# Optimization experiments

Hardware: AMD Instinct MI355X
Metric: run time of the kernel (lower is better)

## Reference

```python
import jax, jax.numpy as jnp
import numpy as np

A_VOCAB = 400000   # embedding table rows (a)
D = 200            # embedding_dim, hard-coded as 200 in the original module
C = 50000          # number of concepts
T = 1000000        # total flattened ancestor entries (~20 per concept)
B = 1024           # batch of input vectors x


def setup_inputs() -> dict:
    key = jax.random.key(0)
    k1, k2, k3, k4 = jax.random.split(key, 4)
    return {
        "x": jax.random.normal(k1, (B, D), dtype=jnp.float32),
        "embed_weight": jax.random.normal(k2, (A_VOCAB, D), dtype=jnp.float32) * 0.02,
        "ancestor_ids": jax.random.randint(k3, (T,), 0, A_VOCAB, dtype=jnp.int32),
        "segment_ids": jnp.sort(jax.random.randint(k4, (T,), 0, C, dtype=jnp.int32)),
        "n_concepts": C,
    }


def reference(x, embed_weight, ancestor_ids, segment_ids, n_concepts):
    # Ragged gather + per-concept sum (the original's Python loop over concepts)
    gathered = embed_weight[ancestor_ids]                                   # [T, D]
    local_H = jax.ops.segment_sum(gathered, segment_ids,
                                  num_segments=n_concepts)                  # [C, D]
    # concept_vector = local_H @ x.T ; output = softmax(concept_vector.T, dim=1)
    logits = jnp.einsum('bd,cd->bc', x, local_H)                            # [B, C]
    return jax.nn.softmax(logits, axis=1)
```

## Files before the change

kernel.cpp:

```cpp
#include <hip/hip_runtime.h>
#include <hip/hip_bf16.h>

#define DDIM   200
#define CSEG   50000
#define TTOT   1000000
#define BROWS  1024
#define KPAD   224
#define NTILE  64
#define NT     782
#define NPAD   50048
#define MTILES 8

typedef __attribute__((ext_vector_type(8))) __bf16 bf16x8;
typedef __attribute__((ext_vector_type(4))) float  f32x4;
typedef unsigned short u16;

#define WS_XB    0
#define WS_HB    458752
#define WS_PART  (458752 + 22421504)
#define WS_INV   (458752 + 22421504 + 3203072)
#define WS_START (458752 + 22421504 + 3203072 + 4096)

__device__ inline u16 f2bf(float f) {
  unsigned u = __float_as_uint(f);
  u += 0x7FFFu + ((u >> 16) & 1u);
  return (u16)(u >> 16);
}

__global__ __launch_bounds__(64) void prep_x_kernel(const float* __restrict__ x,
                                                    u16* __restrict__ xb) {
  const int row = blockIdx.x;
  const int lane = threadIdx.x;
  if (lane >= 56) return;
  const int col = lane * 4;
  ushort4 o = make_ushort4(0, 0, 0, 0);
  if (col < DDIM) {
    const float4 v = *reinterpret_cast<const float4*>(x + (size_t)row * DDIM + col);
    o = make_ushort4(f2bf(v.x), f2bf(v.y), f2bf(v.z), f2bf(v.w));
  }
  *reinterpret_cast<ushort4*>(xb + (size_t)row * KPAD + col) = o;
}

__global__ __launch_bounds__(256) void seg_start_kernel(const int* __restrict__ sid,
                                                        int* __restrict__ start) {
  const int t = blockIdx.x * 256 + threadIdx.x;
  if (t >= TTOT) return;
  const int cur = sid[t];
  const int prev = (t == 0) ? -1 : sid[t - 1];
  for (int c = prev + 1; c <= cur; ++c) start[c] = t;
  if (t == TTOT - 1) {
    for (int c = cur + 1; c <= CSEG; ++c) start[c] = TTOT;
  }
}

__global__ __launch_bounds__(256) void seg_sum_kernel(const float* __restrict__ embed,
                                                      const int* __restrict__ aid,
                                                      const int* __restrict__ start,
                                                      u16* __restrict__ Hb) {
  const int wave = threadIdx.x >> 6;
  const int lane = threadIdx.x & 63;
  const int c = blockIdx.x * 4 + wave;
  if (c >= NPAD || lane >= 56) return;
  const int col = lane * 4;
  const bool act = (col < DDIM);
  float4 a0 = {0.f, 0.f, 0.f, 0.f}, a1 = a0, a2 = a0, a3 = a0;
  if (c < CSEG && act) {
    const int s = start[c], e = start[c + 1];
    int t = s;
    for (; t + 4 <= e; t += 4) {
      const int i0 = aid[t], i1 = aid[t + 1], i2 = aid[t + 2], i3 = aid[t + 3];
      const float4 v0 = *reinterpret_cast<const float4*>(embed + (size_t)i0 * DDIM + col);
      const float4 v1 = *reinterpret_cast<const float4*>(embed + (size_t)i1 * DDIM + col);
      const float4 v2 = *reinterpret_cast<const float4*>(embed + (size_t)i2 * DDIM + col);
      const float4 v3 = *reinterpret_cast<const float4*>(embed + (size_t)i3 * DDIM + col);
      a0.x += v0.x; a0.y += v0.y; a0.z += v0.z; a0.w += v0.w;
      a1.x += v1.x; a1.y += v1.y; a1.z += v1.z; a1.w += v1.w;
      a2.x += v2.x; a2.y += v2.y; a2.z += v2.z; a2.w += v2.w;
      a3.x += v3.x; a3.y += v3.y; a3.z += v3.z; a3.w += v3.w;
    }
    for (; t < e; ++t) {
      const int i0 = aid[t];
      const float4 v0 = *reinterpret_cast<const float4*>(embed + (size_t)i0 * DDIM + col);
      a0.x += v0.x; a0.y += v0.y; a0.z += v0.z; a0.w += v0.w;
    }
    a0.x += a1.x + a2.x + a3.x;
    a0.y += a1.y + a2.y + a3.y;
    a0.z += a1.z + a2.z + a3.z;
    a0.w += a1.w + a2.w + a3.w;
  }
  const ushort4 o = make_ushort4(f2bf(a0.x), f2bf(a0.y), f2bf(a0.z), f2bf(a0.w));
  *reinterpret_cast<ushort4*>(Hb + (size_t)c * KPAD + col) =
      (c < CSEG && act) ? o : make_ushort4(0, 0, 0, 0);
}

__device__ inline void gemm_tile(const u16* __restrict__ xb, const u16* __restrict__ Hb,
                                 int m0, int n0, int lane, f32x4 acc[2][4]) {
  const int r  = lane & 15;
  const int ko = (lane >> 4) * 8;
  const u16* xp = xb + (size_t)(m0 + r) * KPAD + ko;
  const u16* hp = Hb + (size_t)(n0 + r) * KPAD + ko;
  for (int ks = 0; ks < KPAD / 32; ++ks) {
    const int kb = ks * 32;
    const bf16x8 a0 = *reinterpret_cast<const bf16x8*>(xp + kb);
    const bf16x8 a1 = *reinterpret_cast<const bf16x8*>(xp + 16 * KPAD + kb);
#pragma unroll
    for (int ni = 0; ni < 4; ++ni) {
      const bf16x8 b = *reinterpret_cast<const bf16x8*>(hp + (size_t)ni * 16 * KPAD + kb);
      acc[0][ni] = __builtin_amdgcn_mfma_f32_16x16x32_bf16(a0, b, acc[0][ni], 0, 0, 0);
      acc[1][ni] = __builtin_amdgcn_mfma_f32_16x16x32_bf16(a1, b, acc[1][ni], 0, 0, 0);
    }
  }
}

__global__ __launch_bounds__(256) void gemm_pass1_kernel(const u16* __restrict__ xb,
                                                         const u16* __restrict__ Hb,
                                                         float* __restrict__ partials) {
  const int ntile = blockIdx.x, mtile = blockIdx.y;
  const int lane = threadIdx.x & 63, wave = threadIdx.x >> 6;
  const int m0 = mtile * 128 + wave * 32;
  const int n0 = ntile * NTILE;
  f32x4 acc[2][4] = {};
  gemm_tile(xb, Hb, m0, n0, lane, acc);
  const int cbase = n0 + (lane & 15);
#pragma unroll
  for (int mi = 0; mi < 2; ++mi) {
#pragma unroll
    for (int rr = 0; rr < 4; ++rr) {
      float s = 0.f;
#pragma unroll
      for (int ni = 0; ni < 4; ++ni) {
        if (cbase + ni * 16 < CSEG) s += __expf(acc[mi][ni][rr]);
      }
      for (int off = 1; off < 16; off <<= 1) s += __shfl_xor(s, off, 64);
      if ((lane & 15) == 0) {
        const int row = m0 + mi * 16 + (lane >> 4) * 4 + rr;
        partials[(size_t)row * NT + ntile] = s;
      }
    }
  }
}

__global__ __launch_bounds__(256) void reduce_kernel(const float* __restrict__ partials,
                                                     float* __restrict__ invs) {
  const int row = blockIdx.x, tid = threadIdx.x;
  float s = 0.f;
  for (int nt = tid; nt < NT; nt += 256) s += partials[(size_t)row * NT + nt];
  __shared__ float sm[256];
  sm[tid] = s;
  __syncthreads();
  for (int st = 128; st > 0; st >>= 1) {
    if (tid < st) sm[tid] += sm[tid + st];
    __syncthreads();
  }
  if (tid == 0) invs[row] = 1.0f / sm[0];
}

__global__ __launch_bounds__(256) void gemm_pass2_kernel(const u16* __restrict__ xb,
                                                         const u16* __restrict__ Hb,
                                                         const float* __restrict__ invs,
                                                         float* __restrict__ out) {
  const int ntile = blockIdx.x, mtile = blockIdx.y;
  const int lane = threadIdx.x & 63, wave = threadIdx.x >> 6;
  const int m0 = mtile * 128 + wave * 32;
  const int n0 = ntile * NTILE;
  f32x4 acc[2][4] = {};
  gemm_tile(xb, Hb, m0, n0, lane, acc);
  const int c0 = n0 + (lane & 15);
#pragma unroll
  for (int mi = 0; mi < 2; ++mi) {
#pragma unroll
    for (int rr = 0; rr < 4; ++rr) {
      const int row = m0 + mi * 16 + (lane >> 4) * 4 + rr;
      const float inv = invs[row];
      float* orow = out + (size_t)row * CSEG;
#pragma unroll
      for (int ni = 0; ni < 4; ++ni) {
        const int col = c0 + ni * 16;
        if (col < CSEG) orow[col] = __expf(acc[mi][ni][rr]) * inv;
      }
    }
  }
}

extern "C" void kernel_launch(void* const* d_in, const int* in_sizes, int n_in,
                              void* d_out, int out_size, void* d_ws, size_t ws_size,
                              hipStream_t stream) {
  const float* x     = (const float*)d_in[0];
  const float* embed = (const float*)d_in[1];
  const int*   aid   = (const int*)d_in[2];
  const int*   sid   = (const int*)d_in[3];

  char* ws = (char*)d_ws;
  u16*   xb       = (u16*)(ws + WS_XB);
  u16*   Hb       = (u16*)(ws + WS_HB);
  float* partials = (float*)(ws + WS_PART);
  float* invs     = (float*)(ws + WS_INV);
  int*   start    = (int*)(ws + WS_START);
  float* out      = (float*)d_out;

  hipLaunchKernelGGL(prep_x_kernel,     dim3(BROWS),            dim3(64),  0, stream, x, xb);
  hipLaunchKernelGGL(seg_start_kernel,  dim3((TTOT + 255) / 256), dim3(256), 0, stream, sid, start);
  hipLaunchKernelGGL(seg_sum_kernel,    dim3(NPAD / 4),         dim3(256), 0, stream, embed, aid, start, Hb);
  hipLaunchKernelGGL(gemm_pass1_kernel, dim3(NT, MTILES),       dim3(256), 0, stream, xb, Hb, partials);
  hipLaunchKernelGGL(reduce_kernel,     dim3(BROWS),            dim3(256), 0, stream, partials, invs);
  hipLaunchKernelGGL(gemm_pass2_kernel, dim3(NT, MTILES),       dim3(256), 0, stream, xb, Hb, invs, out);
}
```

Baseline: 325.9 us.

## Fuse prep kernels, widen gather unroll, remap GEMM blocks, nontemporal output stores

Merges the x-to-bf16 conversion and the segment-start computation into one launch. The segment-sum gather is unrolled to eight masked loads in flight to add memory-level parallelism. GEMM blocks are remapped over a 1-D grid so that consecutive blocks spread across M tiles in an XCD-aware order. Pass-2 writes its output with nontemporal stores to avoid cache pollution. The masked loads spend extra bandwidth on tail iterations, and the remap may hurt L2 reuse of H tiles.

```diff
diff --git a/kernel.cpp b/kernel.cpp
--- a/kernel.cpp
+++ b/kernel.cpp
@@ -10,6 +10,7 @@
 #define NT     782
 #define NPAD   50048
 #define MTILES 8
+#define GEMM_BLOCKS (NT * MTILES)
 
 typedef __attribute__((ext_vector_type(8))) __bf16 bf16x8;
 typedef __attribute__((ext_vector_type(4))) float  f32x4;
@@ -27,29 +28,28 @@
   return (u16)(u >> 16);
 }
 
-__global__ __launch_bounds__(64) void prep_x_kernel(const float* __restrict__ x,
-                                                    u16* __restrict__ xb) {
-  const int row = blockIdx.x;
-  const int lane = threadIdx.x;
-  if (lane >= 56) return;
-  const int col = lane * 4;
-  ushort4 o = make_ushort4(0, 0, 0, 0);
-  if (col < DDIM) {
-    const float4 v = *reinterpret_cast<const float4*>(x + (size_t)row * DDIM + col);
-    o = make_ushort4(f2bf(v.x), f2bf(v.y), f2bf(v.z), f2bf(v.w));
-  }
-  *reinterpret_cast<ushort4*>(xb + (size_t)row * KPAD + col) = o;
-}
-
-__global__ __launch_bounds__(256) void seg_start_kernel(const int* __restrict__ sid,
-                                                        int* __restrict__ start) {
-  const int t = blockIdx.x * 256 + threadIdx.x;
-  if (t >= TTOT) return;
-  const int cur = sid[t];
-  const int prev = (t == 0) ? -1 : sid[t - 1];
-  for (int c = prev + 1; c <= cur; ++c) start[c] = t;
-  if (t == TTOT - 1) {
-    for (int c = cur + 1; c <= CSEG; ++c) start[c] = TTOT;
+__global__ __launch_bounds__(256) void fused_prep_kernel(const int* __restrict__ sid,
+                                                         int* __restrict__ start,
+                                                         const float* __restrict__ x,
+                                                         u16* __restrict__ xb) {
+  const int gtid = blockIdx.x * 256 + threadIdx.x;
+  if (gtid < TTOT) {
+    const int cur = sid[gtid];
+    const int prev = (gtid == 0) ? -1 : sid[gtid - 1];
+    for (int c = prev + 1; c <= cur; ++c) start[c] = gtid;
+    if (gtid == TTOT - 1) {
+      for (int c = cur + 1; c <= CSEG; ++c) start[c] = TTOT;
+    }
+  }
+  if (gtid < BROWS * 56) {
+    const int row = gtid / 56;
+    const int col = (gtid % 56) * 4;
+    ushort4 o = make_ushort4(0, 0, 0, 0);
+    if (col < DDIM) {
+      const float4 v = *reinterpret_cast<const float4*>(x + (size_t)row * DDIM + col);
+      o = make_ushort4(f2bf(v.x), f2bf(v.y), f2bf(v.z), f2bf(v.w));
+    }
+    *reinterpret_cast<ushort4*>(xb + (size_t)row * KPAD + col) = o;
   }
 }
 
@@ -63,34 +63,51 @@
   if (c >= NPAD || lane >= 56) return;
   const int col = lane * 4;
   const bool act = (col < DDIM);
-  float4 a0 = {0.f, 0.f, 0.f, 0.f}, a1 = a0, a2 = a0, a3 = a0;
+  float4 a[8];
+#pragma unroll
+  for (int j = 0; j < 8; ++j) a[j] = make_float4(0.f, 0.f, 0.f, 0.f);
   if (c < CSEG && act) {
     const int s = start[c], e = start[c + 1];
-    int t = s;
-    for (; t + 4 <= e; t += 4) {
-      const int i0 = aid[t], i1 = aid[t + 1], i2 = aid[t + 2], i3 = aid[t + 3];
-      const float4 v0 = *reinterpret_cast<const float4*>(embed + (size_t)i0 * DDIM + col);
-      const float4 v1 = *reinterpret_cast<const float4*>(embed + (size_t)i1 * DDIM + col);
-      const float4 v2 = *reinterpret_cast<const float4*>(embed + (size_t)i2 * DDIM + col);
-      const float4 v3 = *reinterpret_cast<const float4*>(embed + (size_t)i3 * DDIM + col);
-      a0.x += v0.x; a0.y += v0.y; a0.z += v0.z; a0.w += v0.w;
-      a1.x += v1.x; a1.y += v1.y; a1.z += v1.z; a1.w += v1.w;
-      a2.x += v2.x; a2.y += v2.y; a2.z += v2.z; a2.w += v2.w;
-      a3.x += v3.x; a3.y += v3.y; a3.z += v3.z; a3.w += v3.w;
-    }
-    for (; t < e; ++t) {
-      const int i0 = aid[t];
-      const float4 v0 = *reinterpret_cast<const float4*>(embed + (size_t)i0 * DDIM + col);
-      a0.x += v0.x; a0.y += v0.y; a0.z += v0.z; a0.w += v0.w;
-    }
-    a0.x += a1.x + a2.x + a3.x;
-    a0.y += a1.y + a2.y + a3.y;
-    a0.z += a1.z + a2.z + a3.z;
-    a0.w += a1.w + a2.w + a3.w;
-  }
-  const ushort4 o = make_ushort4(f2bf(a0.x), f2bf(a0.y), f2bf(a0.z), f2bf(a0.w));
-  *reinterpret_cast<ushort4*>(Hb + (size_t)c * KPAD + col) =
-      (c < CSEG && act) ? o : make_ushort4(0, 0, 0, 0);
+    for (int t = s; t < e; t += 8) {
+      int   idx[8];
+      float msk[8];
+#pragma unroll
+      for (int j = 0; j < 8; ++j) {
+        const int tt = t + j;
+        const bool ok = (tt < e);
+        idx[j] = aid[ok ? tt : s];
+        msk[j] = ok ? 1.f : 0.f;
+      }
+#pragma unroll
+      for (int j = 0; j < 8; ++j) {
+        const float4 v = *reinterpret_cast<const float4*>(
+            embed + (size_t)idx[j] * DDIM + col);
+        a[j].x = fmaf(msk[j], v.x, a[j].x);
+        a[j].y = fmaf(msk[j], v.y, a[j].y);
+        a[j].z = fmaf(msk[j], v.z, a[j].z);
+        a[j].w = fmaf(msk[j], v.w, a[j].w);
+      }
+    }
+#pragma unroll
+    for (int j = 4; j < 8; ++j) {
+      a[j - 4].x += a[j].x; a[j - 4].y += a[j].y;
+      a[j - 4].z += a[j].z; a[j - 4].w += a[j].w;
+    }
+    a[0].x += a[1].x + a[2].x + a[3].x;
+    a[0].y += a[1].y + a[2].y + a[3].y;
+    a[0].z += a[1].z + a[2].z + a[3].z;
+    a[0].w += a[1].w + a[2].w + a[3].w;
+  }
+  const ushort4 o = (c < CSEG && act)
+      ? make_ushort4(f2bf(a[0].x), f2bf(a[0].y), f2bf(a[0].z), f2bf(a[0].w))
+      : make_ushort4(0, 0, 0, 0);
+  *reinterpret_cast<ushort4*>(Hb + (size_t)c * KPAD + col) = o;
+}
+
+__device__ inline void gemm_block_map(int orig, int* ntile, int* mtile) {
+  const int f = (orig & 7) * (GEMM_BLOCKS / 8) + (orig >> 3);
+  *ntile = f >> 3;
+  *mtile = f & 7;
 }
 
 __device__ inline void gemm_tile(const u16* __restrict__ xb, const u16* __restrict__ Hb,
@@ -115,7 +132,8 @@
 __global__ __launch_bounds__(256) void gemm_pass1_kernel(const u16* __restrict__ xb,
                                                          const u16* __restrict__ Hb,
                                                          float* __restrict__ partials) {
-  const int ntile = blockIdx.x, mtile = blockIdx.y;
+  int ntile, mtile;
+  gemm_block_map(blockIdx.x, &ntile, &mtile);
   const int lane = threadIdx.x & 63, wave = threadIdx.x >> 6;
   const int m0 = mtile * 128 + wave * 32;
   const int n0 = ntile * NTILE;
@@ -159,7 +177,8 @@
                                                          const u16* __restrict__ Hb,
                                                          const float* __restrict__ invs,
                                                          float* __restrict__ out) {
-  const int ntile = blockIdx.x, mtile = blockIdx.y;
+  int ntile, mtile;
+  gemm_block_map(blockIdx.x, &ntile, &mtile);
   const int lane = threadIdx.x & 63, wave = threadIdx.x >> 6;
   const int m0 = mtile * 128 + wave * 32;
   const int n0 = ntile * NTILE;
@@ -176,7 +195,9 @@
 #pragma unroll
       for (int ni = 0; ni < 4; ++ni) {
         const int col = c0 + ni * 16;
-        if (col < CSEG) orow[col] = __expf(acc[mi][ni][rr]) * inv;
+        if (col < CSEG) {
+          __builtin_nontemporal_store(__expf(acc[mi][ni][rr]) * inv, &orow[col]);
+        }
       }
     }
   }
@@ -198,10 +219,14 @@
   int*   start    = (int*)(ws + WS_START);
   float* out      = (float*)d_out;
 
-  hipLaunchKernelGGL(prep_x_kernel,     dim3(BROWS),            dim3(64),  0, stream, x, xb);
-  hipLaunchKernelGGL(seg_start_kernel,  dim3((TTOT + 255) / 256), dim3(256), 0, stream, sid, start);
-  hipLaunchKernelGGL(seg_sum_kernel,    dim3(NPAD / 4),         dim3(256), 0, stream, embed, aid, start, Hb);
-  hipLaunchKernelGGL(gemm_pass1_kernel, dim3(NT, MTILES),       dim3(256), 0, stream, xb, Hb, partials);
-  hipLaunchKernelGGL(reduce_kernel,     dim3(BROWS),            dim3(256), 0, stream, partials, invs);
-  hipLaunchKernelGGL(gemm_pass2_kernel, dim3(NT, MTILES),       dim3(256), 0, stream, xb, Hb, invs, out);
-}
+  hipLaunchKernelGGL(fused_prep_kernel, dim3((TTOT + 255) / 256), dim3(256), 0, stream,
+                     sid, start, x, xb);
+  hipLaunchKernelGGL(seg_sum_kernel,    dim3(NPAD / 4),    dim3(256), 0, stream,
+                     embed, aid, start, Hb);
+  hipLaunchKernelGGL(gemm_pass1_kernel, dim3(GEMM_BLOCKS), dim3(256), 0, stream,
+                     xb, Hb, partials);
+  hipLaunchKernelGGL(reduce_kernel,     dim3(BROWS),       dim3(256), 0, stream,
+                     partials, invs);
+  hipLaunchKernelGGL(gemm_pass2_kernel, dim3(GEMM_BLOCKS), dim3(256), 0, stream,
+                     xb, Hb, invs, out);
+}
```

Result: faster. 318.5 us (-2.3%).
